# Performance work log

Hardware: AMD Instinct MI355X
Metric: run time of the kernel (lower is better)

Reference implementation:

```python
import jax, jax.numpy as jnp
import numpy as np
from jax import lax

B, CIN, H, W = 64, 256, 56, 56
WIDTH = 64            # bottleneck width (planes * base_width/64 * groups)
COUT = 256            # planes * expansion
SP_BUDGET = 0.5       # spatial budget
CH_BUDGET = 0.5       # channel budget
K_SP = int(SP_BUDGET * H * W)    # 1568 kept pixels
K_CH = int(CH_BUDGET * WIDTH)    # 32 kept channels
EPS = 1e-5


def _conv(x, w, stride=1, pad=0):
    return lax.conv_general_dilated(
        x, w, (stride, stride), [(pad, pad), (pad, pad)],
        dimension_numbers=('NCHW', 'OIHW', 'NCHW'))


def _bn(x, g, b, m, v):
    scale = g / jnp.sqrt(v + EPS)
    return x * scale[None, :, None, None] + (b - m * scale)[None, :, None, None]


def setup_inputs() -> dict:
    key = jax.random.key(0)
    ks = jax.random.split(key, 6)
    inp = {
        'x': jax.random.normal(ks[0], (B, CIN, H, W), jnp.float32),
        'conv1_w': jax.random.normal(ks[1], (WIDTH, CIN, 1, 1), jnp.float32) * 0.05,
        'bn1_g': jnp.ones((WIDTH,), jnp.float32), 'bn1_b': jnp.zeros((WIDTH,), jnp.float32),
        'bn1_m': jnp.zeros((WIDTH,), jnp.float32), 'bn1_v': jnp.ones((WIDTH,), jnp.float32),
        'conv2_w': jax.random.normal(ks[2], (WIDTH, WIDTH, 3, 3), jnp.float32) * 0.05,
        'bn2_g': jnp.ones((WIDTH,), jnp.float32), 'bn2_b': jnp.zeros((WIDTH,), jnp.float32),
        'bn2_m': jnp.zeros((WIDTH,), jnp.float32), 'bn2_v': jnp.ones((WIDTH,), jnp.float32),
        'conv3_w': jax.random.normal(ks[3], (COUT, WIDTH, 1, 1), jnp.float32) * 0.05,
        'bn3_g': jnp.ones((COUT,), jnp.float32), 'bn3_b': jnp.zeros((COUT,), jnp.float32),
        'bn3_m': jnp.zeros((COUT,), jnp.float32), 'bn3_v': jnp.ones((COUT,), jnp.float32),
        'fc_w': jax.random.normal(ks[4], (WIDTH, CIN), jnp.float32) * 0.05,
        'fc_b': jnp.zeros((WIDTH,), jnp.float32),
        'mask_w': jax.random.normal(ks[5], (1, CIN, 1, 1), jnp.float32) * 0.05,
        'mask_b': jnp.zeros((1,), jnp.float32),
    }
    return inp


def reference(x, conv1_w, bn1_g, bn1_b, bn1_m, bn1_v,
              conv2_w, bn2_g, bn2_b, bn2_m, bn2_v,
              conv3_w, bn3_g, bn3_b, bn3_m, bn3_v,
              fc_w, fc_b, mask_w, mask_b):
    identity = x

    # --- ChannelVectorUnit: pooled fc saliency -> hard channel-budget top-k mask [B, WIDTH]
    pooled = x.mean(axis=(2, 3))                         # [B, CIN]
    ch_sal = jax.nn.sigmoid(pooled @ fc_w.T + fc_b)      # [B, WIDTH]
    ch_kth = lax.top_k(ch_sal, K_CH)[0][:, -1:]          # [B, 1]
    vector = (ch_sal >= ch_kth).astype(x.dtype)          # hard 0/1

    # --- MaskUnit: 1x1-conv spatial saliency -> hard spatial-budget top-k mask [B,1,H,W]
    sp_sal = _conv(x, mask_w) + mask_b[None, :, None, None]   # [B,1,H,W]
    sp_flat = sp_sal.reshape(B, H * W)
    sp_kth = lax.top_k(sp_flat, K_SP)[0][:, -1:]
    mask = (sp_flat >= sp_kth).astype(x.dtype).reshape(B, 1, H, W)
    # dilated mask: 3x3 max-dilation (receptive field of the 3x3 conv)
    mask_dilate = lax.reduce_window(mask, 0.0, lax.max, (1, 1, 3, 3), (1, 1, 1, 1), 'SAME')

    # --- masked bottleneck (dense compute, mask multiplies; stride = 1)
    out = _conv(x, conv1_w)
    out = jax.nn.relu(_bn(out, bn1_g, bn1_b, bn1_m, bn1_v)) * mask_dilate
    out = out * vector[:, :, None, None]                 # channel pruning
    out = _conv(out, conv2_w, stride=1, pad=1)
    out = jax.nn.relu(_bn(out, bn2_g, bn2_b, bn2_m, bn2_v)) * mask
    out = out * vector[:, :, None, None]
    out = _conv(out, conv3_w)
    out = _bn(out, bn3_g, bn3_b, bn3_m, bn3_v) * mask
    out = jax.nn.relu(identity + out)
    return out
```

## Files before the change

kernel.cpp:

```cpp
#include <hip/hip_runtime.h>
#include <math.h>

#define BATCH 64
#define CIN   256
#define HH    56
#define WW    56
#define HW    (HH*WW)
#define WIDTH 64
#define COUT  256
#define K_CH  32
#define K_SP  1568
#define EPS   1e-5f

typedef short short8 __attribute__((ext_vector_type(8)));
typedef float f32x4 __attribute__((ext_vector_type(4)));

#define MFMA16(a, b, c) __builtin_amdgcn_mfma_f32_16x16x32_bf16((a), (b), (c), 0, 0, 0)

__device__ __forceinline__ unsigned short f2bf(float f) {
    unsigned u = __builtin_bit_cast(unsigned, f);
    u += 0x7fffu + ((u >> 16) & 1u);
    return (unsigned short)(u >> 16);
}

__global__ __launch_bounds__(256) void k_poolsal(const float* __restrict__ x,
                                                 const float* __restrict__ mask_w,
                                                 double* __restrict__ pooled,
                                                 double* __restrict__ spart) {
    int ct = blockIdx.x, b = blockIdx.y;
    int tid = threadIdx.x;
    __shared__ double pl[16][257];
    double sp0[4], sp1[4], sp2[4], spt[4];
#pragma unroll
    for (int k = 0; k < 4; k++) { sp0[k] = 0.0; sp1[k] = 0.0; sp2[k] = 0.0; spt[k] = 0.0; }

#pragma clang loop unroll(disable)
    for (int c = 0; c < 16; c++) {
        const float* xr = x + ((size_t)(b * CIN + ct * 16 + c)) * HW;
        double w = (double)mask_w[ct * 16 + c];
        f32x4 v0 = *(const f32x4*)(xr + tid * 4);
        f32x4 v1 = *(const f32x4*)(xr + 1024 + tid * 4);
        f32x4 v2 = *(const f32x4*)(xr + 2048 + tid * 4);
        double s = 0.0;
#pragma unroll
        for (int k = 0; k < 4; k++) {
            double d0 = (double)v0[k], d1 = (double)v1[k], d2 = (double)v2[k];
            sp0[k] += d0 * w; sp1[k] += d1 * w; sp2[k] += d2 * w;
            s += d0 + d1 + d2;
        }
        if (tid < 16) {
            f32x4 v3 = *(const f32x4*)(xr + 3072 + tid * 4);
#pragma unroll
            for (int k = 0; k < 4; k++) {
                double d3 = (double)v3[k];
                spt[k] += d3 * w;
                s += d3;
            }
        }
        pl[c][tid] = s;
    }
    double* so = spart + ((size_t)(b * 16 + ct)) * HW;
#pragma unroll
    for (int k = 0; k < 4; k++) {
        so[tid * 4 + k] = sp0[k];
        so[1024 + tid * 4 + k] = sp1[k];
        so[2048 + tid * 4 + k] = sp2[k];
    }
    if (tid < 16) {
#pragma unroll
        for (int k = 0; k < 4; k++) so[3072 + tid * 4 + k] = spt[k];
    }
    __syncthreads();
    for (int off = 128; off > 0; off >>= 1) {
        for (int k = tid; k < 16 * off; k += 256) {
            int c = k / off, j = k - c * off;
            pl[c][j] += pl[c][j + off];
        }
        __syncthreads();
    }
    if (tid < 16) pooled[b * CIN + ct * 16 + tid] = pl[tid][0] * (1.0 / (double)HW);
}

__global__ __launch_bounds__(256) void k_sel(const double* __restrict__ pooled,
                                             const float* __restrict__ fc_w,
                                             const float* __restrict__ fc_b,
                                             const float* __restrict__ w2,
                                             const float* __restrict__ w3,
                                             const double* __restrict__ spart,
                                             float* __restrict__ vector,
                                             int* __restrict__ kidx,
                                             short* __restrict__ wt2c,
                                             short* __restrict__ w3c,
                                             float* __restrict__ mask,
                                             float* __restrict__ mdil) {
    int role = blockIdx.x >> 6;
    int b = blockIdx.x & 63;
    int tid = threadIdx.x;

    __shared__ unsigned long long ks[HW];
    __shared__ float m[HW];
    __shared__ unsigned int hist[256];
    __shared__ unsigned int wsum[4];
    __shared__ unsigned long long sh_prefix;
    __shared__ unsigned int sh_krem;
    __shared__ double ps[CIN];
    __shared__ double ss[WIDTH];
    __shared__ double kth;
    __shared__ int ki[K_CH];

    if (role == 1) {
        for (int i = tid; i < CIN; i += 256) ps[i] = pooled[b * CIN + i];
        __syncthreads();
        if (tid < 64) {
            double acc = (double)fc_b[tid];
            const float* wr = fc_w + tid * CIN;
            for (int k = 0; k < CIN; k++) acc += ps[k] * (double)wr[k];
            ss[tid] = 1.0 / (1.0 + exp(-acc));
        }
        __syncthreads();
        if (tid < 64) {
            double sal = ss[tid];
            int cg = 0, ce = 0;
            for (int i = 0; i < WIDTH; i++) {
                cg += (ss[i] > sal);
                ce += (ss[i] == sal);
            }
            if (cg <= K_CH - 1 && cg + ce >= K_CH) kth = sal;
        }
        __syncthreads();
        if (tid < 64) {
            double sal = ss[tid];
            int kept = (sal >= kth) ? 1 : 0;
            vector[b * WIDTH + tid] = (float)kept;
            int pos = 0;
            for (int i = 0; i < tid; i++) pos += (ss[i] >= kth) ? 1 : 0;
            if (kept && pos < K_CH) { kidx[b * K_CH + pos] = tid; ki[pos] = tid; }
        }
        __syncthreads();
        for (int i = tid; i < 9216; i += 256) {
            int tap = i >> 10, rem = i & 1023;
            int oc_c = rem >> 5, c_c = rem & 31;
            wt2c[(size_t)b * 9216 + i] = (short)f2bf(w2[ki[oc_c] * 576 + ki[c_c] * 9 + tap]);
        }
        for (int i = tid; i < 8192; i += 256) {
            int oc = i >> 5, c_c = i & 31;
            w3c[(size_t)b * 8192 + i] = (short)f2bf(w3[oc * 64 + ki[c_c]]);
        }
        return;
    }

#pragma unroll
    for (int i = 0; i < 13; i++) {
        int px = i * 256 + tid;
        if (px < HW) {
            double s = 0.0;
#pragma unroll
            for (int t = 0; t < 16; t++) s += spart[((size_t)(b * 16 + t)) * HW + px];
            unsigned long long u = __builtin_bit_cast(unsigned long long, s);
            ks[px] = (u >> 63) ? ~u : (u | 0x8000000000000000ULL);
        }
    }
    if (tid == 0) { sh_prefix = 0ULL; sh_krem = K_SP; }
    __syncthreads();

    unsigned long long pmask = 0ULL;
    for (int pass = 0; pass < 8; pass++) {
        int shift = 56 - 8 * pass;
        hist[tid] = 0;
        __syncthreads();
        unsigned long long prefix = sh_prefix;
#pragma unroll
        for (int i = 0; i < 13; i++) {
            int px = i * 256 + tid;
            if (px < HW) {
                unsigned long long k = ks[px];
                if ((k & pmask) == prefix)
                    atomicAdd(&hist[(unsigned)((k >> shift) & 255ULL)], 1u);
            }
        }
        __syncthreads();
        unsigned hval = hist[255 - tid];
        unsigned v = hval;
#pragma unroll
        for (int off2 = 1; off2 < 64; off2 <<= 1) {
            unsigned n = __shfl_up(v, off2, 64);
            if ((tid & 63) >= off2) v += n;
        }
        if ((tid & 63) == 63) wsum[tid >> 6] = v;
        __syncthreads();
        unsigned add = 0;
#pragma unroll
        for (int k2 = 0; k2 < 3; k2++) if ((tid >> 6) > k2) add += wsum[k2];
        v += add;
        unsigned krem = sh_krem;
        unsigned cum = v;
        unsigned cumHigher = v - hval;
        __syncthreads();
        if (cum >= krem && cumHigher < krem) {
            int d = 255 - tid;
            sh_krem = krem - cumHigher;
            sh_prefix = prefix | ((unsigned long long)d << shift);
        }
        pmask |= (0xFFULL << shift);
        __syncthreads();
    }
    unsigned long long kthk = sh_prefix;

#pragma unroll
    for (int i = 0; i < 13; i++) {
        int px = i * 256 + tid;
        if (px < HW) {
            float mv = (ks[px] >= kthk) ? 1.0f : 0.0f;
            m[px] = mv;
            mask[b * HW + px] = mv;
        }
    }
    __syncthreads();
    for (int p = tid; p < HW; p += 256) {
        int y = p / WW, xx = p % WW;
        float mx = 0.0f;
        for (int dy = -1; dy <= 1; dy++) {
            int yy = y + dy;
            if (yy < 0 || yy >= HH) continue;
            for (int dx = -1; dx <= 1; dx++) {
                int xc = xx + dx;
                if (xc < 0 || xc >= WW) continue;
                mx = fmaxf(mx, m[yy * WW + xc]);
            }
        }
        mdil[b * HW + p] = mx;
    }
}

__global__ __launch_bounds__(256, 2) void k_conv1(const float* __restrict__ x,
                                                  const float* __restrict__ w1,
                                                  const float* __restrict__ g1, const float* __restrict__ b1,
                                                  const float* __restrict__ m1, const float* __restrict__ v1,
                                                  const float* __restrict__ mdil,
                                                  const int* __restrict__ kidx,
                                                  short* __restrict__ out1c) {
    __shared__ float scc[32], shc[32];
    __shared__ int ki[32];
    int b = blockIdx.y, p0 = blockIdx.x * 448;
    int tid = threadIdx.x, w = tid >> 6, lane = tid & 63, g = lane >> 4, ln = lane & 15;
    if (tid < 32) {
        int c = kidx[b * K_CH + tid];
        ki[tid] = c;
        float s = g1[c] * rsqrtf(v1[c] + EPS);
        scc[tid] = s; shc[tid] = b1[c] - m1[c] * s;
    }
    __syncthreads();

    int pxw = p0 + w * 112 + ln;
    f32x4 acc[2][7];
    f32x4 zz = {0.f, 0.f, 0.f, 0.f};
#pragma unroll
    for (int m = 0; m < 2; m++)
#pragma unroll
        for (int nt = 0; nt < 7; nt++) acc[m][nt] = zz;

#pragma unroll
    for (int ks = 0; ks < 8; ks++) {
        short8 afr[2];
#pragma unroll
        for (int m = 0; m < 2; m++) {
            const float* wp = w1 + (ki[m * 16 + ln] * 256 + ks * 32 + g * 8);
            f32x4 a0 = *(const f32x4*)(wp);
            f32x4 a1 = *(const f32x4*)(wp + 4);
#pragma unroll
            for (int j = 0; j < 4; j++) {
                afr[m][j]     = (short)f2bf(a0[j]);
                afr[m][4 + j] = (short)f2bf(a1[j]);
            }
        }
        const float* xp0 = x + ((size_t)(b * 256 + ks * 32 + g * 8)) * HW + pxw;
#pragma unroll
        for (int nt = 0; nt < 7; nt++) {
            const float* xp = xp0 + nt * 16;
            short8 bfr;
#pragma unroll
            for (int j = 0; j < 8; j++)
                bfr[j] = (short)f2bf(xp[(size_t)j * HW]);
#pragma unroll
            for (int m = 0; m < 2; m++) acc[m][nt] = MFMA16(afr[m], bfr, acc[m][nt]);
        }
    }
#pragma unroll
    for (int nt = 0; nt < 7; nt++) {
        int px = pxw + nt * 16;
        float md = mdil[b * HW + px];
#pragma unroll
        for (int m = 0; m < 2; m++) {
            int oc = m * 16 + g * 4;
            float y0 = fmaxf(acc[m][nt][0] * scc[oc + 0] + shc[oc + 0], 0.f) * md;
            float y1 = fmaxf(acc[m][nt][1] * scc[oc + 1] + shc[oc + 1], 0.f) * md;
            float y2 = fmaxf(acc[m][nt][2] * scc[oc + 2] + shc[oc + 2], 0.f) * md;
            float y3 = fmaxf(acc[m][nt][3] * scc[oc + 3] + shc[oc + 3], 0.f) * md;
            uint2 u;
            u.x = (unsigned)f2bf(y0) | ((unsigned)f2bf(y1) << 16);
            u.y = (unsigned)f2bf(y2) | ((unsigned)f2bf(y3) << 16);
            *(uint2*)(out1c + ((size_t)(b * HW + px)) * 32 + oc) = u;
        }
    }
}

__global__ __launch_bounds__(128, 2) void k_conv2(const short* __restrict__ out1c,
                                                  const short* __restrict__ wt2c,
                                                  const float* __restrict__ g2, const float* __restrict__ b2,
                                                  const float* __restrict__ m2, const float* __restrict__ v2,
                                                  const float* __restrict__ mask,
                                                  const int* __restrict__ kidx,
                                                  short* __restrict__ out2c) {
    __shared__ short lds[6 * 58 * 32];
    __shared__ float scc[32], shc[32];
    int b = blockIdx.y, r0 = blockIdx.x * 4, p0 = r0 * 56;
    int tid = threadIdx.x, w = tid >> 6, lane = tid & 63, g = lane >> 4, ln = lane & 15;
    if (tid < 32) {
        int c = kidx[b * K_CH + tid];
        float s = g2[c] * rsqrtf(v2[c] + EPS);
        scc[tid] = s; shc[tid] = b2[c] - m2[c] * s;
    }
    short8 z8 = {0, 0, 0, 0, 0, 0, 0, 0};
    for (int i = tid; i < 1392; i += 128) {
        int cblk = i & 3;
        int colr = i >> 2;
        int col = colr % 58, ri = colr / 58;
        int gr = r0 - 1 + ri, gc = col - 1;
        short8 v8 = z8;
        if (gr >= 0 && gr < HH && gc >= 0 && gc < WW)
            v8 = *(const short8*)(out1c + ((size_t)(b * HW + gr * WW + gc)) * 32 + cblk * 8);
        *(short8*)(&lds[(ri * 58 + col) * 32 + ((cblk * 8) ^ ((col & 3) << 3))]) = v8;
    }
    __syncthreads();

    f32x4 acc[2][7];
    f32x4 zz = {0.f, 0.f, 0.f, 0.f};
#pragma unroll
    for (int m = 0; m < 2; m++)
#pragma unroll
        for (int nt = 0; nt < 7; nt++) acc[m][nt] = zz;

    const short* wtb = wt2c + (size_t)b * 9216;
    int prel0 = w * 112 + ln;
    for (int tap = 0; tap < 9; tap++) {
        int dy = tap / 3 - 1;
        int dx = tap - (tap / 3) * 3 - 1;
        short8 afr[2];
#pragma unroll
        for (int m = 0; m < 2; m++)
            afr[m] = *(const short8*)(wtb + tap * 1024 + (m * 16 + ln) * 32 + g * 8);
#pragma unroll
        for (int nt = 0; nt < 7; nt++) {
            int prel = prel0 + nt * 16;
            int rrel = prel / 56;
            int xcol = prel - rrel * 56;
            int row_l = rrel + 1 + dy;
            int col_l = xcol + 1 + dx;
            short8 bfr = *(const short8*)(&lds[(row_l * 58 + col_l) * 32 + ((g * 8) ^ ((col_l & 3) << 3))]);
#pragma unroll
            for (int m = 0; m < 2; m++) acc[m][nt] = MFMA16(afr[m], bfr, acc[m][nt]);
        }
    }
#pragma unroll
    for (int nt = 0; nt < 7; nt++) {
        int px = p0 + prel0 + nt * 16;
        float mv = mask[b * HW + px];
#pragma unroll
        for (int m = 0; m < 2; m++) {
            int oc = m * 16 + g * 4;
            float y0 = fmaxf(acc[m][nt][0] * scc[oc + 0] + shc[oc + 0], 0.f) * mv;
            float y1 = fmaxf(acc[m][nt][1] * scc[oc + 1] + shc[oc + 1], 0.f) * mv;
            float y2 = fmaxf(acc[m][nt][2] * scc[oc + 2] + shc[oc + 2], 0.f) * mv;
            float y3 = fmaxf(acc[m][nt][3] * scc[oc + 3] + shc[oc + 3], 0.f) * mv;
            uint2 u;
            u.x = (unsigned)f2bf(y0) | ((unsigned)f2bf(y1) << 16);
            u.y = (unsigned)f2bf(y2) | ((unsigned)f2bf(y3) << 16);
            *(uint2*)(out2c + ((size_t)(b * HW + px)) * 32 + oc) = u;
        }
    }
}

__global__ __launch_bounds__(256, 4) void k_conv3(const short* __restrict__ out2c,
                                                  const short* __restrict__ w3c,
                                                  const float* __restrict__ g3, const float* __restrict__ b3,
                                                  const float* __restrict__ m3, const float* __restrict__ v3,
                                                  const float* __restrict__ mask,
                                                  const float* __restrict__ x,
                                                  float* __restrict__ out) {
    int b = blockIdx.y;
    int ocb = blockIdx.x / 28;
    int pxb = blockIdx.x % 28;
    int p0 = pxb * 112;
    int tid = threadIdx.x, w = tid >> 6, lane = tid & 63, g = lane >> 4, ln = lane & 15;
    int oc0 = ocb * 64 + w * 16;
    int oc = oc0 + ln;

    const short* w3b = w3c + (size_t)b * 8192;
    short8 wfr = *(const short8*)(w3b + oc * 32 + g * 8);

    short8 act[7];
#pragma unroll
    for (int nt = 0; nt < 7; nt++)
        act[nt] = *(const short8*)(out2c + ((size_t)(b * HW + p0 + nt * 16 + ln)) * 32 + g * 8);

    f32x4 xr[7];
#pragma unroll
    for (int nt = 0; nt < 7; nt++) {
        int px0 = p0 + nt * 16 + g * 4;
        xr[nt] = *(const f32x4*)(x + ((size_t)(b * COUT + oc)) * HW + px0);
    }
    __builtin_amdgcn_sched_barrier(0);

    f32x4 acc[7];
    f32x4 zz = {0.f, 0.f, 0.f, 0.f};
#pragma unroll
    for (int nt = 0; nt < 7; nt++) acc[nt] = zz;
#pragma unroll
    for (int nt = 0; nt < 7; nt++)
        acc[nt] = MFMA16(act[nt], wfr, acc[nt]);

    float s_ = g3[oc] * rsqrtf(v3[oc] + EPS);
    float h_ = b3[oc] - m3[oc] * s_;
#pragma unroll
    for (int nt = 0; nt < 7; nt++) {
        int px0 = p0 + nt * 16 + g * 4;
        f32x4 mv = *(const f32x4*)(mask + (size_t)b * HW + px0);
        size_t idx = ((size_t)(b * COUT + oc)) * HW + px0;
        f32x4 o;
#pragma unroll
        for (int i = 0; i < 4; i++)
            o[i] = fmaxf(xr[nt][i] + (acc[nt][i] * s_ + h_) * mv[i], 0.f);
        *(f32x4*)(out + idx) = o;
    }
}

extern "C" void kernel_launch(void* const* d_in, const int* in_sizes, int n_in,
                              void* d_out, int out_size, void* d_ws, size_t ws_size,
                              hipStream_t stream) {
    const float* x       = (const float*)d_in[0];
    const float* conv1_w = (const float*)d_in[1];
    const float* bn1_g   = (const float*)d_in[2];
    const float* bn1_b   = (const float*)d_in[3];
    const float* bn1_m   = (const float*)d_in[4];
    const float* bn1_v   = (const float*)d_in[5];
    const float* conv2_w = (const float*)d_in[6];
    const float* bn2_g   = (const float*)d_in[7];
    const float* bn2_b   = (const float*)d_in[8];
    const float* bn2_m   = (const float*)d_in[9];
    const float* bn2_v   = (const float*)d_in[10];
    const float* conv3_w = (const float*)d_in[11];
    const float* bn3_g   = (const float*)d_in[12];
    const float* bn3_b   = (const float*)d_in[13];
    const float* bn3_m   = (const float*)d_in[14];
    const float* bn3_v   = (const float*)d_in[15];
    const float* fc_w    = (const float*)d_in[16];
    const float* fc_b    = (const float*)d_in[17];
    const float* mask_w  = (const float*)d_in[18];
    const float* mask_b  = (const float*)d_in[19];
    (void)mask_b;

    char* wsb = (char*)d_ws;
    size_t off = 0;
    double* pooled = (double*)(wsb + off); off += (size_t)BATCH * CIN * 8;
    double* spart  = (double*)(wsb + off); off += (size_t)BATCH * 16 * HW * 8;
    float* vector  = (float*)(wsb + off);  off += (size_t)BATCH * WIDTH * 4;
    float* mask    = (float*)(wsb + off);  off += (size_t)BATCH * HW * 4;
    float* mdil    = (float*)(wsb + off);  off += (size_t)BATCH * HW * 4;
    int*   kidx    = (int*)(wsb + off);    off += (size_t)BATCH * K_CH * 4;
    short* wt2c    = (short*)(wsb + off);  off += (size_t)BATCH * 9216 * 2;
    short* w3c     = (short*)(wsb + off);  off += (size_t)BATCH * 8192 * 2;
    short* out1c   = (short*)(wsb + off);  off += (size_t)BATCH * HW * 32 * 2;
    short* out2c   = (short*)(wsb + off);  off += (size_t)BATCH * HW * 32 * 2;
    (void)ws_size; (void)in_sizes; (void)n_in; (void)out_size; (void)vector;

    k_poolsal<<<dim3(16, BATCH), 256, 0, stream>>>(x, mask_w, pooled, spart);
    k_sel<<<128, 256, 0, stream>>>(pooled, fc_w, fc_b, conv2_w, conv3_w, spart,
                                   vector, kidx, wt2c, w3c, mask, mdil);
    k_conv1<<<dim3(7, BATCH), 256, 0, stream>>>(x, conv1_w, bn1_g, bn1_b, bn1_m, bn1_v, mdil, kidx, out1c);
    k_conv2<<<dim3(14, BATCH), 128, 0, stream>>>(out1c, wt2c, bn2_g, bn2_b, bn2_m, bn2_v, mask, kidx, out2c);
    k_conv3<<<dim3(112, BATCH), 256, 0, stream>>>(out2c, w3c, bn3_g, bn3_b, bn3_m, bn3_v, mask, x, (float*)d_out);
}
```

Before: 212.3 us.

## Fuse conv2 and conv3 into one kernel, keeping conv2 output in LDS

Merges the 3x3 conv2 kernel and the 1x1 conv3 kernel so conv2's bf16 output is written to the reused LDS tile with a swizzle instead of a global buffer. conv3 then loops over 16 output-channel groups per block, reading activations from LDS and doing the residual add and store. This removes the out2c round trip through global memory and one kernel launch. In exchange the conv3 and epilogue stage now runs on only 14x64 blocks of 128 threads, which is far less parallelism than the old 112x64 grid of 256-thread blocks, so the x/out streaming of this memory-bound stage may be less well overlapped.

```diff
diff --git a/kernel.cpp b/kernel.cpp
--- a/kernel.cpp
+++ b/kernel.cpp
@@ -304,21 +304,32 @@
     }
 }
 
-__global__ __launch_bounds__(128, 2) void k_conv2(const short* __restrict__ out1c,
-                                                  const short* __restrict__ wt2c,
-                                                  const float* __restrict__ g2, const float* __restrict__ b2,
-                                                  const float* __restrict__ m2, const float* __restrict__ v2,
-                                                  const float* __restrict__ mask,
-                                                  const int* __restrict__ kidx,
-                                                  short* __restrict__ out2c) {
-    __shared__ short lds[6 * 58 * 32];
+__global__ __launch_bounds__(128, 2) void k_conv23(const short* __restrict__ out1c,
+                                                   const short* __restrict__ wt2c,
+                                                   const float* __restrict__ g2, const float* __restrict__ b2,
+                                                   const float* __restrict__ m2, const float* __restrict__ v2,
+                                                   const short* __restrict__ w3c,
+                                                   const float* __restrict__ g3, const float* __restrict__ b3,
+                                                   const float* __restrict__ m3, const float* __restrict__ v3,
+                                                   const float* __restrict__ mask,
+                                                   const int* __restrict__ kidx,
+                                                   const float* __restrict__ x,
+                                                   float* __restrict__ out) {
+    __shared__ short tile[6 * 58 * 32];
     __shared__ float scc[32], shc[32];
+    __shared__ float sc3[COUT], sh3[COUT];
     int b = blockIdx.y, r0 = blockIdx.x * 4, p0 = r0 * 56;
     int tid = threadIdx.x, w = tid >> 6, lane = tid & 63, g = lane >> 4, ln = lane & 15;
     if (tid < 32) {
         int c = kidx[b * K_CH + tid];
         float s = g2[c] * rsqrtf(v2[c] + EPS);
         scc[tid] = s; shc[tid] = b2[c] - m2[c] * s;
+    }
+#pragma unroll
+    for (int r = 0; r < 2; r++) {
+        int oc = r * 128 + tid;
+        float s = g3[oc] * rsqrtf(v3[oc] + EPS);
+        sc3[oc] = s; sh3[oc] = b3[oc] - m3[oc] * s;
     }
     short8 z8 = {0, 0, 0, 0, 0, 0, 0, 0};
     for (int i = tid; i < 1392; i += 128) {
@@ -329,7 +340,7 @@
         short8 v8 = z8;
         if (gr >= 0 && gr < HH && gc >= 0 && gc < WW)
             v8 = *(const short8*)(out1c + ((size_t)(b * HW + gr * WW + gc)) * 32 + cblk * 8);
-        *(short8*)(&lds[(ri * 58 + col) * 32 + ((cblk * 8) ^ ((col & 3) << 3))]) = v8;
+        *(short8*)(&tile[(ri * 58 + col) * 32 + ((cblk * 8) ^ ((col & 3) << 3))]) = v8;
     }
     __syncthreads();
 
@@ -356,15 +367,17 @@
             int xcol = prel - rrel * 56;
             int row_l = rrel + 1 + dy;
             int col_l = xcol + 1 + dx;
-            short8 bfr = *(const short8*)(&lds[(row_l * 58 + col_l) * 32 + ((g * 8) ^ ((col_l & 3) << 3))]);
+            short8 bfr = *(const short8*)(&tile[(row_l * 58 + col_l) * 32 + ((g * 8) ^ ((col_l & 3) << 3))]);
 #pragma unroll
             for (int m = 0; m < 2; m++) acc[m][nt] = MFMA16(afr[m], bfr, acc[m][nt]);
         }
     }
+    __syncthreads();
+
 #pragma unroll
     for (int nt = 0; nt < 7; nt++) {
-        int px = p0 + prel0 + nt * 16;
-        float mv = mask[b * HW + px];
+        int loc = prel0 + nt * 16;
+        float mv = mask[b * HW + p0 + loc];
 #pragma unroll
         for (int m = 0; m < 2; m++) {
             int oc = m * 16 + g * 4;
@@ -375,62 +388,42 @@
             uint2 u;
             u.x = (unsigned)f2bf(y0) | ((unsigned)f2bf(y1) << 16);
             u.y = (unsigned)f2bf(y2) | ((unsigned)f2bf(y3) << 16);
-            *(uint2*)(out2c + ((size_t)(b * HW + px)) * 32 + oc) = u;
-        }
-    }
-}
-
-__global__ __launch_bounds__(256, 4) void k_conv3(const short* __restrict__ out2c,
-                                                  const short* __restrict__ w3c,
-                                                  const float* __restrict__ g3, const float* __restrict__ b3,
-                                                  const float* __restrict__ m3, const float* __restrict__ v3,
-                                                  const float* __restrict__ mask,
-                                                  const float* __restrict__ x,
-                                                  float* __restrict__ out) {
-    int b = blockIdx.y;
-    int ocb = blockIdx.x / 28;
-    int pxb = blockIdx.x % 28;
-    int p0 = pxb * 112;
-    int tid = threadIdx.x, w = tid >> 6, lane = tid & 63, g = lane >> 4, ln = lane & 15;
-    int oc0 = ocb * 64 + w * 16;
-    int oc = oc0 + ln;
-
+            int chunk = m * 2 + (g >> 1);
+            int soff = loc * 32 + ((chunk ^ ((loc >> 1) & 3)) << 3) + ((g & 1) << 2);
+            *(uint2*)(&tile[soff]) = u;
+        }
+    }
+    __syncthreads();
+
+    short8 act[7];
+#pragma unroll
+    for (int nt = 0; nt < 7; nt++) {
+        int loc = w * 112 + nt * 16 + ln;
+        act[nt] = *(const short8*)(&tile[loc * 32 + ((g ^ ((loc >> 1) & 3)) << 3)]);
+    }
     const short* w3b = w3c + (size_t)b * 8192;
-    short8 wfr = *(const short8*)(w3b + oc * 32 + g * 8);
-
-    short8 act[7];
-#pragma unroll
-    for (int nt = 0; nt < 7; nt++)
-        act[nt] = *(const short8*)(out2c + ((size_t)(b * HW + p0 + nt * 16 + ln)) * 32 + g * 8);
-
-    f32x4 xr[7];
-#pragma unroll
-    for (int nt = 0; nt < 7; nt++) {
-        int px0 = p0 + nt * 16 + g * 4;
-        xr[nt] = *(const f32x4*)(x + ((size_t)(b * COUT + oc)) * HW + px0);
-    }
-    __builtin_amdgcn_sched_barrier(0);
-
-    f32x4 acc[7];
-    f32x4 zz = {0.f, 0.f, 0.f, 0.f};
-#pragma unroll
-    for (int nt = 0; nt < 7; nt++) acc[nt] = zz;
-#pragma unroll
-    for (int nt = 0; nt < 7; nt++)
-        acc[nt] = MFMA16(act[nt], wfr, acc[nt]);
-
-    float s_ = g3[oc] * rsqrtf(v3[oc] + EPS);
-    float h_ = b3[oc] - m3[oc] * s_;
-#pragma unroll
-    for (int nt = 0; nt < 7; nt++) {
-        int px0 = p0 + nt * 16 + g * 4;
-        f32x4 mv = *(const f32x4*)(mask + (size_t)b * HW + px0);
-        size_t idx = ((size_t)(b * COUT + oc)) * HW + px0;
-        f32x4 o;
-#pragma unroll
-        for (int i = 0; i < 4; i++)
-            o[i] = fmaxf(xr[nt][i] + (acc[nt][i] * s_ + h_) * mv[i], 0.f);
-        *(f32x4*)(out + idx) = o;
+#pragma clang loop unroll(disable)
+    for (int mo = 0; mo < 16; mo++) {
+        int oc = mo * 16 + ln;
+        short8 wfr = *(const short8*)(w3b + oc * 32 + g * 8);
+        f32x4 a7[7];
+#pragma unroll
+        for (int nt = 0; nt < 7; nt++) a7[nt] = zz;
+#pragma unroll
+        for (int nt = 0; nt < 7; nt++) a7[nt] = MFMA16(act[nt], wfr, a7[nt]);
+        float s_ = sc3[oc], h_ = sh3[oc];
+#pragma unroll
+        for (int nt = 0; nt < 7; nt++) {
+            int px0 = p0 + w * 112 + nt * 16 + g * 4;
+            f32x4 mv = *(const f32x4*)(mask + (size_t)b * HW + px0);
+            size_t idx = ((size_t)(b * COUT + oc)) * HW + px0;
+            f32x4 xr = *(const f32x4*)(x + idx);
+            f32x4 o;
+#pragma unroll
+            for (int i = 0; i < 4; i++)
+                o[i] = fmaxf(xr[i] + (a7[nt][i] * s_ + h_) * mv[i], 0.f);
+            *(f32x4*)(out + idx) = o;
+        }
     }
 }
 
@@ -470,13 +463,13 @@
     short* wt2c    = (short*)(wsb + off);  off += (size_t)BATCH * 9216 * 2;
     short* w3c     = (short*)(wsb + off);  off += (size_t)BATCH * 8192 * 2;
     short* out1c   = (short*)(wsb + off);  off += (size_t)BATCH * HW * 32 * 2;
-    short* out2c   = (short*)(wsb + off);  off += (size_t)BATCH * HW * 32 * 2;
     (void)ws_size; (void)in_sizes; (void)n_in; (void)out_size; (void)vector;
 
     k_poolsal<<<dim3(16, BATCH), 256, 0, stream>>>(x, mask_w, pooled, spart);
     k_sel<<<128, 256, 0, stream>>>(pooled, fc_w, fc_b, conv2_w, conv3_w, spart,
                                    vector, kidx, wt2c, w3c, mask, mdil);
     k_conv1<<<dim3(7, BATCH), 256, 0, stream>>>(x, conv1_w, bn1_g, bn1_b, bn1_m, bn1_v, mdil, kidx, out1c);
-    k_conv2<<<dim3(14, BATCH), 128, 0, stream>>>(out1c, wt2c, bn2_g, bn2_b, bn2_m, bn2_v, mask, kidx, out2c);
-    k_conv3<<<dim3(112, BATCH), 256, 0, stream>>>(out2c, w3c, bn3_g, bn3_b, bn3_m, bn3_v, mask, x, (float*)d_out);
-}
+    k_conv23<<<dim3(14, BATCH), 128, 0, stream>>>(out1c, wt2c, bn2_g, bn2_b, bn2_m, bn2_v,
+                                                  w3c, bn3_g, bn3_b, bn3_m, bn3_v,
+                                                  mask, kidx, x, (float*)d_out);
+}
```

After: 217.4 us. +2.4%, slower.
